# Performance work log

Measured on AMD Instinct MI355X. Metric: run time of the kernel, lower is better.

## Reference

```python
import jax, jax.numpy as jnp
import numpy as np

D_MODEL = 1024
N_HEADS = 16
SPARSITY_FACTOR = 4  # band half-width
HEAD_DIM = D_MODEL // N_HEADS
SCALE = HEAD_DIM ** (-0.5)


def _band_mask(seq_len: int, stride: int) -> jnp.ndarray:
    # mask[i, j] = True iff max(0, i-stride) <= j <= min(S-1, i+stride)
    i = jnp.arange(seq_len)[:, None]
    j = jnp.arange(seq_len)[None, :]
    return jnp.abs(i - j) <= stride


def setup_inputs() -> dict:
    key = jax.random.key(0)
    kq, kk, kv = jax.random.split(key, 3)
    B, S = 256, 128
    q = jax.random.normal(kq, (B, S, D_MODEL), dtype=jnp.float32)
    k = jax.random.normal(kk, (B, S, D_MODEL), dtype=jnp.float32)
    v = jax.random.normal(kv, (B, S, D_MODEL), dtype=jnp.float32)
    return {"q": q, "k": k, "v": v}


def reference(q, k, v):
    B, S, _ = q.shape
    # [B, S, D] -> [B, H, S, Dh]
    qh = q.reshape(B, S, N_HEADS, HEAD_DIM).transpose(0, 2, 1, 3)
    kh = k.reshape(B, S, N_HEADS, HEAD_DIM).transpose(0, 2, 1, 3)
    vh = v.reshape(B, S, N_HEADS, HEAD_DIM).transpose(0, 2, 1, 3)
    # dense scores, then banded mask (faithful to original)
    scores = jnp.einsum("bhqd,bhkd->bhqk", qh, kh) * SCALE  # [B,H,S,S]
    mask = _band_mask(S, SPARSITY_FACTOR)  # [S,S] bool
    scores = jnp.where(mask, scores, -jnp.inf)
    weights = jax.nn.softmax(scores, axis=-1)
    out = jnp.einsum("bhqk,bhkd->bhqd", weights, vh)  # [B,H,S,Dh]
    return out.transpose(0, 2, 1, 3).reshape(B, S, D_MODEL)
```

## Files before the change

kernel.cpp:

```cpp
#include <hip/hip_runtime.h>

#define SEQ   128
#define DM    1024
#define NH    16
#define HD    64
#define BAND  4
#define WIN   9
#define SCALE 0.125f

__device__ __forceinline__ float allreduce16(float x) {
#define DPP_ADD(ctrl)                                                          \
  x += __int_as_float(                                                         \
      __builtin_amdgcn_update_dpp(0, __float_as_int(x), ctrl, 0xf, 0xf, true));
  DPP_ADD(0xB1)
  DPP_ADD(0x4E)
  DPP_ADD(0x124)
  DPP_ADD(0x128)
#undef DPP_ADD
  return x;
}

__global__ __launch_bounds__(256, 4)
void banded_attn(const float* __restrict__ q, const float* __restrict__ k,
                 const float* __restrict__ v, float* __restrict__ out) {
  const int lane = threadIdx.x & 63;
  const int wid  = (blockIdx.x << 2) | (threadIdx.x >> 6);
  const int half = wid & 1;
  const int bh   = wid >> 1;
  const int h    = bh & (NH - 1);
  const int b    = bh >> 4;

  const int g = lane >> 4;
  const int l = lane & 15;

  const size_t base = (size_t)b * (SEQ * DM) + (size_t)h * HD + 4 * l;
  const float* qb = q + base;
  const float* kb = k + base;
  const float* vb = v + base;
  float*       ob = out + base;

  const int i0 = half * 64;

  for (int s = 0; s < 16; ++s) {
    const int iq = i0 + 4 * s + g;
    const float4 q4 = *reinterpret_cast<const float4*>(qb + (size_t)iq * DM);

    float  sum = 0.f;
    float4 o4  = {0.f, 0.f, 0.f, 0.f};
#pragma unroll
    for (int t = 0; t < WIN; ++t) {
      const int j  = iq - BAND + t;
      const int jc = min(max(j, 0), SEQ - 1);
      const float4 k4 = *reinterpret_cast<const float4*>(kb + (size_t)jc * DM);
      const float4 v4 = *reinterpret_cast<const float4*>(vb + (size_t)jc * DM);

      const float p = q4.x * k4.x + q4.y * k4.y + q4.z * k4.z + q4.w * k4.w;
      const float r = allreduce16(p);

      const float e = ((unsigned)j < SEQ) ? __expf(r * SCALE) : 0.f;
      sum += e;
      o4.x += e * v4.x; o4.y += e * v4.y; o4.z += e * v4.z; o4.w += e * v4.w;
    }

    const float inv = __builtin_amdgcn_rcpf(sum);
    float4 r4 = {o4.x * inv, o4.y * inv, o4.z * inv, o4.w * inv};
    *reinterpret_cast<float4*>(ob + (size_t)iq * DM) = r4;
  }
}

extern "C" void kernel_launch(void* const* d_in, const int* in_sizes, int n_in,
                              void* d_out, int out_size, void* d_ws, size_t ws_size,
                              hipStream_t stream) {
  const float* q = (const float*)d_in[0];
  const float* k = (const float*)d_in[1];
  const float* v = (const float*)d_in[2];
  float* out = (float*)d_out;

  dim3 grid(2048), block(256);
  hipLaunchKernelGGL(banded_attn, grid, block, 0, stream, q, k, v, out);
}
```

Before: 470.5 us.

## Keep sliding K/V window in registers and prefetch next rows

Each 16-lane group now holds its 9-row K/V window in registers and slides it by 4 rows per step, loading only the 4 new rows instead of all 9. The next step's K/V and Q rows are loaded before the current step's math so their latency is overlapped. Q is prescaled by scale*log2(e) so the softmax can use exp2, and boundary masking is applied only on the first and last steps. The extra register use is covered by lowering the launch bound occupancy from 4 to 3 blocks per SIMD, which may reduce latency hiding.

```diff
diff --git a/kernel.cpp b/kernel.cpp
--- a/kernel.cpp
+++ b/kernel.cpp
@@ -7,6 +7,7 @@
 #define BAND  4
 #define WIN   9
 #define SCALE 0.125f
+#define SCALE_LOG2E 0.18033688011112042f
 
 __device__ __forceinline__ float allreduce16(float x) {
 #define DPP_ADD(ctrl)                                                          \
@@ -20,7 +21,7 @@
   return x;
 }
 
-__global__ __launch_bounds__(256, 4)
+__global__ __launch_bounds__(256, 3)
 void banded_attn(const float* __restrict__ q, const float* __restrict__ k,
                  const float* __restrict__ v, float* __restrict__ out) {
   const int lane = threadIdx.x & 63;
@@ -39,32 +40,69 @@
   const float* vb = v + base;
   float*       ob = out + base;
 
-  const int i0 = half * 64;
+  const int i0  = half * 64;
+  const int iq0 = i0 + g;
 
+  float4 kw[WIN], vw[WIN];
+#pragma unroll
+  for (int t = 0; t < WIN; ++t) {
+    const int j  = iq0 - BAND + t;
+    const int jc = min(max(j, 0), SEQ - 1);
+    kw[t] = *reinterpret_cast<const float4*>(kb + (size_t)jc * DM);
+    vw[t] = *reinterpret_cast<const float4*>(vb + (size_t)jc * DM);
+  }
+
+  float4 q4 = *reinterpret_cast<const float4*>(qb + (size_t)iq0 * DM);
+  q4.x *= SCALE_LOG2E; q4.y *= SCALE_LOG2E;
+  q4.z *= SCALE_LOG2E; q4.w *= SCALE_LOG2E;
+
+#pragma unroll
   for (int s = 0; s < 16; ++s) {
     const int iq = i0 + 4 * s + g;
-    const float4 q4 = *reinterpret_cast<const float4*>(qb + (size_t)iq * DM);
+
+    float4 nk[4], nv[4], nq;
+    if (s < 15) {
+#pragma unroll
+      for (int u = 0; u < 4; ++u) {
+        const int j  = iq + BAND + 1 + u;
+        const int jc = min(j, SEQ - 1);
+        nk[u] = *reinterpret_cast<const float4*>(kb + (size_t)jc * DM);
+        nv[u] = *reinterpret_cast<const float4*>(vb + (size_t)jc * DM);
+      }
+      nq = *reinterpret_cast<const float4*>(qb + (size_t)(iq + 4) * DM);
+    }
 
     float  sum = 0.f;
     float4 o4  = {0.f, 0.f, 0.f, 0.f};
 #pragma unroll
     for (int t = 0; t < WIN; ++t) {
-      const int j  = iq - BAND + t;
-      const int jc = min(max(j, 0), SEQ - 1);
-      const float4 k4 = *reinterpret_cast<const float4*>(kb + (size_t)jc * DM);
-      const float4 v4 = *reinterpret_cast<const float4*>(vb + (size_t)jc * DM);
-
-      const float p = q4.x * k4.x + q4.y * k4.y + q4.z * k4.z + q4.w * k4.w;
+      const int j = iq - BAND + t;
+      const float p =
+          q4.x * kw[t].x + q4.y * kw[t].y + q4.z * kw[t].z + q4.w * kw[t].w;
       const float r = allreduce16(p);
-
-      const float e = ((unsigned)j < SEQ) ? __expf(r * SCALE) : 0.f;
+      float e;
+      if (s == 0 || s == 15) {
+        e = ((unsigned)j < SEQ) ? __builtin_amdgcn_exp2f(r) : 0.f;
+      } else {
+        e = __builtin_amdgcn_exp2f(r);
+      }
       sum += e;
-      o4.x += e * v4.x; o4.y += e * v4.y; o4.z += e * v4.z; o4.w += e * v4.w;
+      o4.x += e * vw[t].x; o4.y += e * vw[t].y;
+      o4.z += e * vw[t].z; o4.w += e * vw[t].w;
     }
 
     const float inv = __builtin_amdgcn_rcpf(sum);
     float4 r4 = {o4.x * inv, o4.y * inv, o4.z * inv, o4.w * inv};
     *reinterpret_cast<float4*>(ob + (size_t)iq * DM) = r4;
+
+    if (s < 15) {
+#pragma unroll
+      for (int t = 0; t < 5; ++t) { kw[t] = kw[t + 4]; vw[t] = vw[t + 4]; }
+#pragma unroll
+      for (int u = 0; u < 4; ++u) { kw[5 + u] = nk[u]; vw[5 + u] = nv[u]; }
+      q4.x = nq.x * SCALE_LOG2E; q4.y = nq.y * SCALE_LOG2E;
+      q4.z = nq.z * SCALE_LOG2E; q4.w = nq.w * SCALE_LOG2E;
+    }
   }
 }
 
```

New measurement: 394.2 us. 16.2% less time.

## Stage banded K/V rows in LDS per block and prefetch Q rows

Applied to the files above, without the earlier changes.

Each block now handles one (batch, head, half) slice with four waves sharing a 72-row K/V window staged cooperatively into padded LDS. This replaces the per-query global reloads of nine K and V rows, which relied on caches for reuse. Q is prefetched one step ahead and pre-scaled by scale*log2e so exp2 can stand in for expf. The grid grows to 8192 blocks with 36KB of LDS each, which may limit occupancy, and a barrier is added after staging.

```diff
diff --git a/kernel.cpp b/kernel.cpp
--- a/kernel.cpp
+++ b/kernel.cpp
@@ -6,7 +6,9 @@
 #define HD    64
 #define BAND  4
 #define WIN   9
-#define SCALE 0.125f
+#define NROWS 72
+#define LDST  68
+#define SCALE_LOG2E 0.18033688011112042f
 
 __device__ __forceinline__ float allreduce16(float x) {
 #define DPP_ADD(ctrl)                                                          \
@@ -23,8 +25,13 @@
 __global__ __launch_bounds__(256, 4)
 void banded_attn(const float* __restrict__ q, const float* __restrict__ k,
                  const float* __restrict__ v, float* __restrict__ out) {
-  const int lane = threadIdx.x & 63;
-  const int wid  = (blockIdx.x << 2) | (threadIdx.x >> 6);
+  __shared__ __align__(16) float klds[NROWS * LDST];
+  __shared__ __align__(16) float vlds[NROWS * LDST];
+
+  const int tid  = threadIdx.x;
+  const int lane = tid & 63;
+  const int w    = tid >> 6;
+  const int wid  = blockIdx.x;
   const int half = wid & 1;
   const int bh   = wid >> 1;
   const int h    = bh & (NH - 1);
@@ -33,38 +40,79 @@
   const int g = lane >> 4;
   const int l = lane & 15;
 
-  const size_t base = (size_t)b * (SEQ * DM) + (size_t)h * HD + 4 * l;
-  const float* qb = q + base;
-  const float* kb = k + base;
-  const float* vb = v + base;
-  float*       ob = out + base;
-
+  const size_t hbase = (size_t)b * (SEQ * DM) + (size_t)h * HD;
   const int i0 = half * 64;
 
-  for (int s = 0; s < 16; ++s) {
-    const int iq = i0 + 4 * s + g;
-    const float4 q4 = *reinterpret_cast<const float4*>(qb + (size_t)iq * DM);
+  const int lq0 = (w << 4) + g;
+  float4 q4 = *reinterpret_cast<const float4*>(
+      q + hbase + (size_t)(i0 + lq0) * DM + 4 * l);
+
+  {
+    float4 kr[5], vr[5];
+#pragma unroll
+    for (int p = 0; p < 5; ++p) {
+      const int idx = tid + (p << 8);
+      const int rr  = idx >> 4;
+      if (rr < NROWS) {
+        const int jr = min(max(i0 - BAND + rr, 0), SEQ - 1);
+        const int c  = (idx & 15) << 2;
+        kr[p] = *reinterpret_cast<const float4*>(k + hbase + (size_t)jr * DM + c);
+        vr[p] = *reinterpret_cast<const float4*>(v + hbase + (size_t)jr * DM + c);
+      }
+    }
+#pragma unroll
+    for (int p = 0; p < 5; ++p) {
+      const int idx = tid + (p << 8);
+      const int rr  = idx >> 4;
+      if (rr < NROWS) {
+        const int c = (idx & 15) << 2;
+        *reinterpret_cast<float4*>(&klds[rr * LDST + c]) = kr[p];
+        *reinterpret_cast<float4*>(&vlds[rr * LDST + c]) = vr[p];
+      }
+    }
+  }
+
+  q4.x *= SCALE_LOG2E; q4.y *= SCALE_LOG2E;
+  q4.z *= SCALE_LOG2E; q4.w *= SCALE_LOG2E;
+  __syncthreads();
+
+#pragma unroll
+  for (int s = 0; s < 4; ++s) {
+    const int lq = (w << 4) + (s << 2) + g;
+    const int iq = i0 + lq;
+
+    float4 nq;
+    if (s < 3)
+      nq = *reinterpret_cast<const float4*>(
+          q + hbase + (size_t)(iq + 4) * DM + 4 * l);
 
     float  sum = 0.f;
     float4 o4  = {0.f, 0.f, 0.f, 0.f};
 #pragma unroll
     for (int t = 0; t < WIN; ++t) {
-      const int j  = iq - BAND + t;
-      const int jc = min(max(j, 0), SEQ - 1);
-      const float4 k4 = *reinterpret_cast<const float4*>(kb + (size_t)jc * DM);
-      const float4 v4 = *reinterpret_cast<const float4*>(vb + (size_t)jc * DM);
-
-      const float p = q4.x * k4.x + q4.y * k4.y + q4.z * k4.z + q4.w * k4.w;
+      const int rr = lq + t;
+      const float4 k4 =
+          *reinterpret_cast<const float4*>(&klds[rr * LDST + 4 * l]);
+      const float4 v4 =
+          *reinterpret_cast<const float4*>(&vlds[rr * LDST + 4 * l]);
+      const float p =
+          q4.x * k4.x + q4.y * k4.y + q4.z * k4.z + q4.w * k4.w;
       const float r = allreduce16(p);
-
-      const float e = ((unsigned)j < SEQ) ? __expf(r * SCALE) : 0.f;
+      const int j = iq - BAND + t;
+      const float e = ((unsigned)j < SEQ) ? __builtin_amdgcn_exp2f(r) : 0.f;
       sum += e;
-      o4.x += e * v4.x; o4.y += e * v4.y; o4.z += e * v4.z; o4.w += e * v4.w;
+      o4.x += e * v4.x; o4.y += e * v4.y;
+      o4.z += e * v4.z; o4.w += e * v4.w;
     }
 
     const float inv = __builtin_amdgcn_rcpf(sum);
     float4 r4 = {o4.x * inv, o4.y * inv, o4.z * inv, o4.w * inv};
-    *reinterpret_cast<float4*>(ob + (size_t)iq * DM) = r4;
+    *reinterpret_cast<float4*>(out + hbase + (size_t)iq * DM + 4 * l) = r4;
+
+    if (s < 3) {
+      q4.x = nq.x * SCALE_LOG2E; q4.y = nq.y * SCALE_LOG2E;
+      q4.z = nq.z * SCALE_LOG2E; q4.w = nq.w * SCALE_LOG2E;
+    }
   }
 }
 
@@ -76,6 +124,6 @@
   const float* v = (const float*)d_in[2];
   float* out = (float*)d_out;
 
-  dim3 grid(2048), block(256);
+  dim3 grid(8192), block(256);
   hipLaunchKernelGGL(banded_attn, grid, block, 0, stream, q, k, v, out);
 }
```

Result: faster. 436.4 us (-7.2%).
